# Kernel tuning notes

Hardware: AMD Instinct MI355X
Metric: run time of the kernel (lower is better)

Reference implementation:

```python
import jax, jax.numpy as jnp
import numpy as np

B, L, D = 32, 256, 128


def hard_sigmoid(x):
    # Keras-1 default inner_activation for LSTM gates
    return jnp.clip(0.2 * x + 0.5, 0.0, 1.0)


def lstm_step(x_t, h, c, W, U, b):
    # Keras-1 gate order: i, f, c(candidate), o
    z = x_t @ W + h @ U + b  # [B, 4D]
    d = h.shape[-1]
    i = hard_sigmoid(z[:, :d])
    f = hard_sigmoid(z[:, d:2 * d])
    g = jnp.tanh(z[:, 2 * d:3 * d])
    o = hard_sigmoid(z[:, 3 * d:])
    c_new = f * c + i * g
    h_new = o * jnp.tanh(c_new)
    return h_new, c_new


def setup_inputs() -> dict:
    key = jax.random.key(0)
    ks = jax.random.split(key, 9)
    s = 0.05  # weight scale to keep activations in a sane range
    return {
        "x": jax.random.normal(ks[0], (B, L, D), dtype=jnp.float32),
        "Wr": jax.random.normal(ks[1], (D, 4 * D), dtype=jnp.float32) * s,
        "Ur": jax.random.normal(ks[2], (D, 4 * D), dtype=jnp.float32) * s,
        "br": jnp.zeros((4 * D,), dtype=jnp.float32),
        "Ww": jax.random.normal(ks[3], (D, 4 * D), dtype=jnp.float32) * s,
        "Uw": jax.random.normal(ks[4], (D, 4 * D), dtype=jnp.float32) * s,
        "bw": jnp.zeros((4 * D,), dtype=jnp.float32),
        "Wc": jax.random.normal(ks[5], (2 * D, D), dtype=jnp.float32) * s,
        "bc": jnp.zeros((D,), dtype=jnp.float32),
    }


def reference(x, Wr, Ur, br, Ww, Uw, bw, Wc, bc):
    b, l, d = x.shape
    h0 = jnp.zeros((b, d), dtype=x.dtype)

    # ---- reader LSTM (return_sequences) ----
    def reader_step(carry, x_t):
        h, c = carry
        h, c = lstm_step(x_t, h, c, Wr, Ur, br)
        return (h, c), h

    _, o_seq = jax.lax.scan(reader_step, (h0, h0), jnp.swapaxes(x, 0, 1))  # [L, B, D]

    # ---- compose-and-write scan over timesteps ----
    mem0 = x  # read() sets mem_0 = input

    def write_step(carry, o_t):
        mem, h, c = carry  # mem: [B, L, D]
        # eq 2-3: attention over memory slots
        z = jax.nn.softmax(jnp.einsum('bd,bld->bl', o_t, mem), axis=-1)  # [B, L]
        m_rt = jnp.einsum('bl,bld->bd', z, mem)  # [B, D]
        # eq 4: composer (linear activation)
        c_t = jnp.concatenate([o_t, m_rt], axis=-1) @ Wc + bc  # [B, D]
        # eq 5: writer LSTM step
        h, c = lstm_step(c_t, h, c, Ww, Uw, bw)
        # eq 6: soft overwrite of memory
        zc = z[:, :, None]
        mem = mem * (1.0 - zc) + h[:, None, :] * zc
        return (mem, h, c), h

    (_, _, _), hs = jax.lax.scan(write_step, (mem0, h0, h0), o_seq)
    # return_mode == 'last_output'
    return hs[-1]
```

## Files before the change

### kernel.cpp

```cpp
#include <hip/hip_runtime.h>
#include <stdint.h>


#define LL 256

typedef float v2f __attribute__((ext_vector_type(2)));

__device__ __forceinline__ float hsig(float x) { return fminf(fmaxf(fmaf(x, 0.2f, 0.5f), 0.f), 1.f); }
__device__ __forceinline__ float tanh_fast(float x) {
  x = fminf(fmaxf(x, -15.f), 15.f);
  float e = __expf(2.f * x);
  return (e - 1.f) / (e + 1.f);
}

__global__ __launch_bounds__(512) void wtrans_kernel(const float* __restrict__ src,
                                                     float* __restrict__ dst, int jshift) {
  int idx = blockIdx.x * 512 + threadIdx.x;
  int J = 1 << jshift;
  int k = idx >> jshift, j = idx & (J - 1);
  dst[(((size_t)(k >> 2) << jshift) + j) * 4 + (k & 3)] = src[idx];
}

__global__ __launch_bounds__(512) void pvw_gemm(const float* __restrict__ Wc,
                                                const float* __restrict__ Ww,
                                                float* __restrict__ PVw) {
  __shared__ float wrow[128];
  const int r = blockIdx.x, j = threadIdx.x;
  if (j < 128) wrow[j] = Wc[r * 128 + j];
  __syncthreads();
  float a = 0.f;
#pragma unroll 4
  for (int m = 0; m < 128; m++) a = fmaf(wrow[m], Ww[m * 512 + j], a);
  PVw[r * 512 + j] = a;
}

__global__ __launch_bounds__(512) void pz_kernel(const float* __restrict__ bc,
                                                 const float* __restrict__ Ww,
                                                 const float* __restrict__ bw,
                                                 float* __restrict__ pz) {
  __shared__ float b_s[128];
  const int j = threadIdx.x;
  if (j < 128) b_s[j] = bc[j];
  __syncthreads();
  float a = bw[j];
#pragma unroll 4
  for (int m = 0; m < 128; m++) a = fmaf(b_s[m], Ww[m * 512 + j], a);
  pz[j] = a;
}

__global__ __launch_bounds__(512) void xw_gemm(const float* __restrict__ x,
                                               const float4* __restrict__ WrT4,
                                               const float* __restrict__ br,
                                               float* __restrict__ XW) {
  alignas(16) __shared__ float xs[8][128];
  const int b = blockIdx.x >> 5, tg = blockIdx.x & 31, tid = threadIdx.x;
  const float* xg = x + ((size_t)b * LL + tg * 8) * 128;
  if (tid < 256) ((float4*)&xs[0][0])[tid] = ((const float4*)xg)[tid];
  __syncthreads();
  float acc[8];
#pragma unroll
  for (int r = 0; r < 8; r++) acc[r] = 0.f;
#pragma unroll 8
  for (int i4 = 0; i4 < 32; i4++) {
    float4 w4 = WrT4[i4 * 512 + tid];
#pragma unroll
    for (int r = 0; r < 8; r++) {
      float4 v = *(const float4*)&xs[r][4 * i4];
      acc[r] += w4.x * v.x + w4.y * v.y + w4.z * v.z + w4.w * v.w;
    }
  }
  const float brj = br[tid];
  float* o = XW + ((size_t)b * LL + tg * 8) * 512;
#pragma unroll
  for (int r = 0; r < 8; r++) o[r * 512 + tid] = acc[r] + brj;
}

__global__ __launch_bounds__(512, 2) void reader_kernel(const float4* __restrict__ UrT4,
                                                        const float* __restrict__ XW,
                                                        float* __restrict__ og) {
  alignas(16) __shared__ float h_s[128];
  alignas(16) __shared__ float pp_s[512];
  const int b = blockIdx.x, tid = threadIdx.x;
  const float* XWb = XW + (size_t)b * LL * 512;
  float* ogb = og + (size_t)b * LL * 128;

  float4 U[32];
#pragma unroll
  for (int i4 = 0; i4 < 32; i4++) U[i4] = UrT4[i4 * 512 + tid];

  float c_r = 0.f;
  if (tid < 128) h_s[tid] = 0.f;
  float xwv = XWb[tid];
  __syncthreads();

  for (int t = 0; t < LL; t++) {
    float xw_n = (t + 1 < LL) ? XWb[(t + 1) * 512 + tid] : 0.f;
    v2f acc[4] = {{0.f, 0.f}, {0.f, 0.f}, {0.f, 0.f}, {0.f, 0.f}};
#pragma unroll
    for (int i4 = 0; i4 < 32; i4++) {
      float4 v = *(const float4*)&h_s[4 * i4];
      float4 w = U[i4];
      acc[i4 & 3] += (v2f){w.x, w.y} * (v2f){v.x, v.y};
      acc[i4 & 3] += (v2f){w.z, w.w} * (v2f){v.z, v.w};
    }
    v2f A = (acc[0] + acc[1]) + (acc[2] + acc[3]);
    pp_s[tid] = A.x + A.y + xwv;
    __syncthreads();
    if (tid < 128) {
      float zi = pp_s[tid], zf = pp_s[128 + tid], zg = pp_s[256 + tid], zo = pp_s[384 + tid];
      float ii = hsig(zi), ff = hsig(zf), gg = tanh_fast(zg), oo = hsig(zo);
      c_r = fmaf(ff, c_r, ii * gg);
      float h = oo * tanh_fast(c_r);
      h_s[tid] = h;
      ogb[t * 128 + tid] = h;
    }
    __syncthreads();
    xwv = xw_n;
  }
}

template <int NC>
__global__ __launch_bounds__(512, 2) void writer_kernel(
    const float* __restrict__ x,
    const float4* __restrict__ VwT4, const float4* __restrict__ UwT4,
    const float* __restrict__ og, const float* __restrict__ ZW,
    float* __restrict__ out) {
  alignas(16) __shared__ float h_s[128];
  alignas(16) __shared__ float osN[128];
  alignas(16) __shared__ float sc_s[256], ee_s[256];
  alignas(16) __shared__ float mr_s[128];
  alignas(16) __shared__ float pp_s[1024];
  __shared__ float rr_s[16];
  extern __shared__ float4 UwL[];

  const int b = blockIdx.x, tid = threadIdx.x;
  const int lane = tid & 63, wv = tid >> 6;
  const int l = tid >> 1, hf = tid & 1;
  const int q = tid >> 6, dp = tid & 63;

  const float* xg = x + (size_t)b * (LL * 128);
  const float* ogb = og + (size_t)b * (LL * 128);
  const float* ZWb = ZW + (size_t)b * (LL * 512);

  for (int i = tid; i < NC * 512; i += 512) UwL[i] = UwT4[i];

  v2f Mr[32], Mc[32];
#pragma unroll
  for (int w = 0; w < 32; w++) Mr[w] = *(const v2f*)(xg + l * 128 + hf * 64 + 2 * w);
#pragma unroll
  for (int i = 0; i < 32; i++) Mc[i] = *(const v2f*)(xg + (q * 32 + i) * 128 + 2 * dp);

  float c_w = 0.f;
  if (tid < 128) { h_s[tid] = 0.f; osN[tid] = ogb[tid]; }
  __syncthreads();
  {
    v2f S = {0.f, 0.f};
#pragma unroll
    for (int w = 0; w < 32; w++) S += Mr[w] * (*(const v2f*)&osN[hf * 64 + 2 * w]);
    float s = S.x + S.y;
    s += __shfl_xor(s, 1);
    if (hf == 0) sc_s[l] = s;
  }
  __syncthreads();

  float zwv = ZWb[tid];
  for (int t = 0; t < LL; t++) {
    const int tn = (t + 1 < LL) ? t + 1 : t;
    float zw_n = ZWb[(size_t)tn * 512 + tid];

    float huv;
    {
      v2f u0 = {0.f, 0.f}, u1 = {0.f, 0.f}, u2 = {0.f, 0.f}, u3 = {0.f, 0.f};
#pragma unroll 2
      for (int i4 = NC; i4 < 32; i4 += 2) {
        float4 w0 = UwT4[i4 * 512 + tid];
        float4 w1 = UwT4[(i4 + 1) * 512 + tid];
        float4 v0 = *(const float4*)&h_s[4 * i4];
        float4 v1 = *(const float4*)&h_s[4 * i4 + 4];
        u0 += (v2f){w0.x, w0.y} * (v2f){v0.x, v0.y};
        u0 += (v2f){w0.z, w0.w} * (v2f){v0.z, v0.w};
        u1 += (v2f){w1.x, w1.y} * (v2f){v1.x, v1.y};
        u1 += (v2f){w1.z, w1.w} * (v2f){v1.z, v1.w};
      }
#pragma unroll 2
      for (int i4 = 0; i4 < NC; i4++) {
        float4 w = UwL[i4 * 512 + tid];
        float4 v = *(const float4*)&h_s[4 * i4];
        u2 += (v2f){w.x, w.y} * (v2f){v.x, v.y};
        u3 += (v2f){w.z, w.w} * (v2f){v.z, v.w};
      }
      v2f U = (u0 + u1) + (u2 + u3);
      huv = U.x + U.y + zwv;
    }

    if (tid >= 128 && tid < 256 && t + 1 < LL)
      osN[tid - 128] = ogb[(t + 1) * 128 + (tid - 128)];
    if (tid < 256) {
      float s = sc_s[tid];
      float m = s;
#pragma unroll
      for (int off = 32; off > 0; off >>= 1) m = fmaxf(m, __shfl_xor(m, off));
      float e = __expf(s - m);
      ee_s[tid] = e;
      float s2 = e;
#pragma unroll
      for (int off = 32; off > 0; off >>= 1) s2 += __shfl_xor(s2, off);
      if (lane == 0) { rr_s[wv] = m; rr_s[8 + wv] = s2; }
    }
    __syncthreads();

    const float M = fmaxf(fmaxf(rr_s[0], rr_s[1]), fmaxf(rr_s[2], rr_s[3]));
    const float Sg = rr_s[8] * __expf(rr_s[0] - M) + rr_s[9] * __expf(rr_s[1] - M) +
                     rr_s[10] * __expf(rr_s[2] - M) + rr_s[11] * __expf(rr_s[3] - M);
    const float inv = 1.f / Sg;
    const float f = __expf(rr_s[tid >> 7] - M);
    const float fzi = f * inv;

    {
      v2f P0 = {0.f, 0.f}, P1 = {0.f, 0.f};
#pragma unroll
      for (int i = 0; i < 32; i += 2) {
        P0 += Mc[i] * ee_s[q * 32 + i];
        P1 += Mc[i + 1] * ee_s[q * 32 + i + 1];
      }
      v2f P = (P0 + P1) * f;
      *(v2f*)&pp_s[q * 128 + 2 * dp] = P;
    }
    __syncthreads();
    if (tid < 128) {
      float s = 0.f;
#pragma unroll
      for (int g8 = 0; g8 < 8; g8++) s += pp_s[g8 * 128 + tid];
      mr_s[tid] = s;
    }
    __syncthreads();
    {
      v2f a0 = {0.f, 0.f}, a1 = {0.f, 0.f}, a2 = {0.f, 0.f}, a3 = {0.f, 0.f};
#pragma unroll 2
      for (int i4 = 0; i4 < 32; i4 += 4) {
        float4 w0 = VwT4[i4 * 512 + tid];
        float4 w1 = VwT4[(i4 + 1) * 512 + tid];
        float4 w2 = VwT4[(i4 + 2) * 512 + tid];
        float4 w3 = VwT4[(i4 + 3) * 512 + tid];
        float4 v0 = *(const float4*)&mr_s[4 * i4];
        float4 v1 = *(const float4*)&mr_s[4 * i4 + 4];
        float4 v2 = *(const float4*)&mr_s[4 * i4 + 8];
        float4 v3 = *(const float4*)&mr_s[4 * i4 + 12];
        a0 += (v2f){w0.x, w0.y} * (v2f){v0.x, v0.y};
        a0 += (v2f){w0.z, w0.w} * (v2f){v0.z, v0.w};
        a1 += (v2f){w1.x, w1.y} * (v2f){v1.x, v1.y};
        a1 += (v2f){w1.z, w1.w} * (v2f){v1.z, v1.w};
        a2 += (v2f){w2.x, w2.y} * (v2f){v2.x, v2.y};
        a2 += (v2f){w2.z, w2.w} * (v2f){v2.z, v2.w};
        a3 += (v2f){w3.x, w3.y} * (v2f){v3.x, v3.y};
        a3 += (v2f){w3.z, w3.w} * (v2f){v3.z, v3.w};
      }
      v2f A = (a0 + a2) + (a1 + a3);
      pp_s[tid] = fmaf(A.x + A.y, inv, huv);
    }
    __syncthreads();
    if (tid < 128) {
      float zi = pp_s[tid], zf = pp_s[128 + tid], zg = pp_s[256 + tid], zo = pp_s[384 + tid];
      float ii = hsig(zi), ff = hsig(zf), gg = tanh_fast(zg), oo = hsig(zo);
      c_w = fmaf(ff, c_w, ii * gg);
      h_s[tid] = oo * tanh_fast(c_w);
    }
    __syncthreads();
    if (t + 1 < LL) {
      const float zr = ee_s[l] * fzi;
      v2f S0v = {0.f, 0.f}, S1v = {0.f, 0.f};
#pragma unroll
      for (int w = 0; w < 32; w += 2) {
        v2f h2a = *(const v2f*)&h_s[hf * 64 + 2 * w];
        v2f ma = Mr[w];
        v2f na = ma + (h2a - ma) * zr;
        Mr[w] = na;
        S0v += na * (*(const v2f*)&osN[hf * 64 + 2 * w]);
        v2f h2b = *(const v2f*)&h_s[hf * 64 + 2 * (w + 1)];
        v2f mb = Mr[w + 1];
        v2f nb = mb + (h2b - mb) * zr;
        Mr[w + 1] = nb;
        S1v += nb * (*(const v2f*)&osN[hf * 64 + 2 * (w + 1)]);
      }
      v2f Sv = S0v + S1v;
      float s = Sv.x + Sv.y;
      s += __shfl_xor(s, 1);
      if (hf == 0) sc_s[l] = s;
      v2f hc = *(const v2f*)&h_s[2 * dp];
#pragma unroll
      for (int i = 0; i < 32; i++) {
        float zc = ee_s[q * 32 + i] * fzi;
        v2f m = Mc[i];
        Mc[i] = m + (hc - m) * zc;
      }
    }
    __syncthreads();
    zwv = zw_n;
  }

  if (tid < 128) out[b * 128 + tid] = h_s[tid];
}

extern "C" void kernel_launch(void* const* d_in, const int* in_sizes, int n_in,
                              void* d_out, int out_size, void* d_ws, size_t ws_size,
                              hipStream_t stream) {
  const float* x  = (const float*)d_in[0];
  const float* Wr = (const float*)d_in[1];
  const float* Ur = (const float*)d_in[2];
  const float* br = (const float*)d_in[3];
  const float* Ww = (const float*)d_in[4];
  const float* Uw = (const float*)d_in[5];
  const float* bw = (const float*)d_in[6];
  const float* Wc = (const float*)d_in[7];
  const float* bc = (const float*)d_in[8];
  float* out = (float*)d_out;

  float* og  = (float*)d_ws;
  float* XW  = og + 1048576;
  float* WrT = XW + 4194304;
  float* UrT = WrT + 65536;
  float* UwT = UrT + 65536;
  float* PVw = UwT + 65536;
  float* PwT = PVw + 131072;
  float* VwT = PwT + 65536;
  float* pz  = VwT + 65536;

  static int nc_cached = -1;
  if (nc_cached < 0) {
    int want = 18 * 512 * (int)sizeof(float4);
    nc_cached = (hipFuncSetAttribute(
                     reinterpret_cast<const void*>(&writer_kernel<18>),
                     hipFuncAttributeMaxDynamicSharedMemorySize, want) == hipSuccess)
                    ? 18
                    : 6;
  }

  wtrans_kernel<<<128, 512, 0, stream>>>(Wr, WrT, 9);
  wtrans_kernel<<<128, 512, 0, stream>>>(Ur, UrT, 9);
  wtrans_kernel<<<128, 512, 0, stream>>>(Uw, UwT, 9);
  pvw_gemm<<<256, 512, 0, stream>>>(Wc, Ww, PVw);
  pz_kernel<<<1, 512, 0, stream>>>(bc, Ww, bw, pz);
  wtrans_kernel<<<128, 512, 0, stream>>>(PVw, PwT, 9);
  wtrans_kernel<<<128, 512, 0, stream>>>(PVw + 65536, VwT, 9);
  xw_gemm<<<1024, 512, 0, stream>>>(x, (const float4*)WrT, br, XW);
  reader_kernel<<<32, 512, 0, stream>>>((const float4*)UrT, XW, og);
  xw_gemm<<<1024, 512, 0, stream>>>(og, (const float4*)PwT, pz, XW);
  if (nc_cached == 18) {
    writer_kernel<18><<<32, 512, 18 * 512 * sizeof(float4), stream>>>(
        x, (const float4*)VwT, (const float4*)UwT, og, XW, out);
  } else {
    writer_kernel<6><<<32, 512, 6 * 512 * sizeof(float4), stream>>>(
        x, (const float4*)VwT, (const float4*)UwT, og, XW, out);
  }
}
```

Baseline: 2.030 ms.

## Move writer memory into padded LDS and keep Uw weights in registers

The writer kernel used to hold the memory matrix twice in registers (a row-major copy and a column-major copy) and kept part of Uw in LDS. It now stores one copy of the memory in dynamic LDS with a padded stride of 130, which frees the registers so the full Uw slice per thread can live in 32 float4 registers. The softmax is also restructured into a two-pass global max, which removes the per-group rescale factors. The trade-off is extra LDS traffic on every timestep for the memory reads and writes, plus one additional barrier, with a fallback kernel kept for cases where the LDS allocation fails.

```diff
diff --git a/kernel.cpp b/kernel.cpp
--- a/kernel.cpp
+++ b/kernel.cpp
@@ -3,6 +3,7 @@
 
 
 #define LL 256
+#define MS 130
 
 typedef float v2f __attribute__((ext_vector_type(2)));
 
@@ -119,8 +120,7 @@
   }
 }
 
-template <int NC>
-__global__ __launch_bounds__(512, 2) void writer_kernel(
+__global__ __launch_bounds__(512, 2) void writer_mem_lds(
     const float* __restrict__ x,
     const float4* __restrict__ VwT4, const float4* __restrict__ UwT4,
     const float* __restrict__ og, const float* __restrict__ ZW,
@@ -131,7 +131,7 @@
   alignas(16) __shared__ float mr_s[128];
   alignas(16) __shared__ float pp_s[1024];
   __shared__ float rr_s[16];
-  extern __shared__ float4 UwL[];
+  extern __shared__ float memL[];
 
   const int b = blockIdx.x, tid = threadIdx.x;
   const int lane = tid & 63, wv = tid >> 6;
@@ -142,21 +142,24 @@
   const float* ogb = og + (size_t)b * (LL * 128);
   const float* ZWb = ZW + (size_t)b * (LL * 512);
 
-  for (int i = tid; i < NC * 512; i += 512) UwL[i] = UwT4[i];
-
-  v2f Mr[32], Mc[32];
-#pragma unroll
-  for (int w = 0; w < 32; w++) Mr[w] = *(const v2f*)(xg + l * 128 + hf * 64 + 2 * w);
-#pragma unroll
-  for (int i = 0; i < 32; i++) Mc[i] = *(const v2f*)(xg + (q * 32 + i) * 128 + 2 * dp);
+  float4 UW[32];
+#pragma unroll
+  for (int i4 = 0; i4 < 32; i4++) UW[i4] = UwT4[i4 * 512 + tid];
+
+  for (int idx = tid; idx < 16384; idx += 512) {
+    int row = idx >> 6, c2 = (idx & 63) << 1;
+    *(v2f*)&memL[row * MS + c2] = *(const v2f*)&xg[(row << 7) + c2];
+  }
 
   float c_w = 0.f;
   if (tid < 128) { h_s[tid] = 0.f; osN[tid] = ogb[tid]; }
   __syncthreads();
   {
+    const float* mrow = &memL[l * MS + hf * 64];
     v2f S = {0.f, 0.f};
 #pragma unroll
-    for (int w = 0; w < 32; w++) S += Mr[w] * (*(const v2f*)&osN[hf * 64 + 2 * w]);
+    for (int w = 0; w < 32; w++)
+      S += (*(const v2f*)&mrow[2 * w]) * (*(const v2f*)&osN[hf * 64 + 2 * w]);
     float s = S.x + S.y;
     s += __shfl_xor(s, 1);
     if (hf == 0) sc_s[l] = s;
@@ -170,60 +173,47 @@
 
     float huv;
     {
-      v2f u0 = {0.f, 0.f}, u1 = {0.f, 0.f}, u2 = {0.f, 0.f}, u3 = {0.f, 0.f};
-#pragma unroll 2
-      for (int i4 = NC; i4 < 32; i4 += 2) {
-        float4 w0 = UwT4[i4 * 512 + tid];
-        float4 w1 = UwT4[(i4 + 1) * 512 + tid];
-        float4 v0 = *(const float4*)&h_s[4 * i4];
-        float4 v1 = *(const float4*)&h_s[4 * i4 + 4];
-        u0 += (v2f){w0.x, w0.y} * (v2f){v0.x, v0.y};
-        u0 += (v2f){w0.z, w0.w} * (v2f){v0.z, v0.w};
-        u1 += (v2f){w1.x, w1.y} * (v2f){v1.x, v1.y};
-        u1 += (v2f){w1.z, w1.w} * (v2f){v1.z, v1.w};
-      }
-#pragma unroll 2
-      for (int i4 = 0; i4 < NC; i4++) {
-        float4 w = UwL[i4 * 512 + tid];
+      v2f acc[4] = {{0.f, 0.f}, {0.f, 0.f}, {0.f, 0.f}, {0.f, 0.f}};
+#pragma unroll
+      for (int i4 = 0; i4 < 32; i4++) {
         float4 v = *(const float4*)&h_s[4 * i4];
-        u2 += (v2f){w.x, w.y} * (v2f){v.x, v.y};
-        u3 += (v2f){w.z, w.w} * (v2f){v.z, v.w};
-      }
-      v2f U = (u0 + u1) + (u2 + u3);
-      huv = U.x + U.y + zwv;
+        float4 w = UW[i4];
+        acc[i4 & 3] += (v2f){w.x, w.y} * (v2f){v.x, v.y};
+        acc[i4 & 3] += (v2f){w.z, w.w} * (v2f){v.z, v.w};
+      }
+      v2f A = (acc[0] + acc[1]) + (acc[2] + acc[3]);
+      huv = A.x + A.y + zwv;
     }
 
     if (tid >= 128 && tid < 256 && t + 1 < LL)
       osN[tid - 128] = ogb[(t + 1) * 128 + (tid - 128)];
     if (tid < 256) {
-      float s = sc_s[tid];
-      float m = s;
+      float m = sc_s[tid];
 #pragma unroll
       for (int off = 32; off > 0; off >>= 1) m = fmaxf(m, __shfl_xor(m, off));
-      float e = __expf(s - m);
+      if (lane == 0) rr_s[wv] = m;
+    }
+    __syncthreads();
+    if (tid < 256) {
+      float mx = fmaxf(fmaxf(rr_s[0], rr_s[1]), fmaxf(rr_s[2], rr_s[3]));
+      float e = __expf(sc_s[tid] - mx);
       ee_s[tid] = e;
       float s2 = e;
 #pragma unroll
       for (int off = 32; off > 0; off >>= 1) s2 += __shfl_xor(s2, off);
-      if (lane == 0) { rr_s[wv] = m; rr_s[8 + wv] = s2; }
-    }
-    __syncthreads();
-
-    const float M = fmaxf(fmaxf(rr_s[0], rr_s[1]), fmaxf(rr_s[2], rr_s[3]));
-    const float Sg = rr_s[8] * __expf(rr_s[0] - M) + rr_s[9] * __expf(rr_s[1] - M) +
-                     rr_s[10] * __expf(rr_s[2] - M) + rr_s[11] * __expf(rr_s[3] - M);
-    const float inv = 1.f / Sg;
-    const float f = __expf(rr_s[tid >> 7] - M);
-    const float fzi = f * inv;
-
+      if (lane == 0) rr_s[8 + wv] = s2;
+    }
+    __syncthreads();
+    const float inv = 1.f / (rr_s[8] + rr_s[9] + rr_s[10] + rr_s[11]);
     {
+      const float* mcol = &memL[(q * 32) * MS + 2 * dp];
       v2f P0 = {0.f, 0.f}, P1 = {0.f, 0.f};
 #pragma unroll
       for (int i = 0; i < 32; i += 2) {
-        P0 += Mc[i] * ee_s[q * 32 + i];
-        P1 += Mc[i + 1] * ee_s[q * 32 + i + 1];
-      }
-      v2f P = (P0 + P1) * f;
+        P0 += (*(const v2f*)&mcol[i * MS]) * ee_s[q * 32 + i];
+        P1 += (*(const v2f*)&mcol[(i + 1) * MS]) * ee_s[q * 32 + i + 1];
+      }
+      v2f P = P0 + P1;
       *(v2f*)&pp_s[q * 128 + 2 * dp] = P;
     }
     __syncthreads();
@@ -231,7 +221,7 @@
       float s = 0.f;
 #pragma unroll
       for (int g8 = 0; g8 < 8; g8++) s += pp_s[g8 * 128 + tid];
-      mr_s[tid] = s;
+      mr_s[tid] = s * inv;
     }
     __syncthreads();
     {
@@ -256,7 +246,7 @@
         a3 += (v2f){w3.z, w3.w} * (v2f){v3.z, v3.w};
       }
       v2f A = (a0 + a2) + (a1 + a3);
-      pp_s[tid] = fmaf(A.x + A.y, inv, huv);
+      pp_s[tid] = A.x + A.y + huv;
     }
     __syncthreads();
     if (tid < 128) {
@@ -267,7 +257,176 @@
     }
     __syncthreads();
     if (t + 1 < LL) {
-      const float zr = ee_s[l] * fzi;
+      const float zr = ee_s[l] * inv;
+      float* mrow = &memL[l * MS + hf * 64];
+      v2f S0v = {0.f, 0.f}, S1v = {0.f, 0.f};
+#pragma unroll
+      for (int w = 0; w < 32; w += 2) {
+        v2f h2a = *(const v2f*)&h_s[hf * 64 + 2 * w];
+        v2f ma = *(const v2f*)&mrow[2 * w];
+        v2f na = ma + (h2a - ma) * zr;
+        *(v2f*)&mrow[2 * w] = na;
+        S0v += na * (*(const v2f*)&osN[hf * 64 + 2 * w]);
+        v2f h2b = *(const v2f*)&h_s[hf * 64 + 2 * (w + 1)];
+        v2f mb = *(const v2f*)&mrow[2 * (w + 1)];
+        v2f nb = mb + (h2b - mb) * zr;
+        *(v2f*)&mrow[2 * (w + 1)] = nb;
+        S1v += nb * (*(const v2f*)&osN[hf * 64 + 2 * (w + 1)]);
+      }
+      v2f Sv = S0v + S1v;
+      float s = Sv.x + Sv.y;
+      s += __shfl_xor(s, 1);
+      if (hf == 0) sc_s[l] = s;
+    }
+    __syncthreads();
+    zwv = zw_n;
+  }
+
+  if (tid < 128) out[b * 128 + tid] = h_s[tid];
+}
+
+template <int NC>
+__global__ __launch_bounds__(512, 2) void writer_fb(
+    const float* __restrict__ x,
+    const float4* __restrict__ VwT4, const float4* __restrict__ UwT4,
+    const float* __restrict__ og, const float* __restrict__ ZW,
+    float* __restrict__ out) {
+  alignas(16) __shared__ float h_s[128];
+  alignas(16) __shared__ float osN[128];
+  alignas(16) __shared__ float sc_s[256], ee_s[256];
+  alignas(16) __shared__ float mr_s[128];
+  alignas(16) __shared__ float pp_s[1024];
+  __shared__ float rr_s[16];
+  extern __shared__ float4 UwL[];
+
+  const int b = blockIdx.x, tid = threadIdx.x;
+  const int lane = tid & 63, wv = tid >> 6;
+  const int l = tid >> 1, hf = tid & 1;
+  const int q = tid >> 6, dp = tid & 63;
+
+  const float* xg = x + (size_t)b * (LL * 128);
+  const float* ogb = og + (size_t)b * (LL * 128);
+  const float* ZWb = ZW + (size_t)b * (LL * 512);
+
+  for (int i = tid; i < NC * 512; i += 512) UwL[i] = UwT4[i];
+
+  v2f Mr[32], Mc[32];
+#pragma unroll
+  for (int w = 0; w < 32; w++) Mr[w] = *(const v2f*)(xg + l * 128 + hf * 64 + 2 * w);
+#pragma unroll
+  for (int i = 0; i < 32; i++) Mc[i] = *(const v2f*)(xg + (q * 32 + i) * 128 + 2 * dp);
+
+  float c_w = 0.f;
+  if (tid < 128) { h_s[tid] = 0.f; osN[tid] = ogb[tid]; }
+  __syncthreads();
+  {
+    v2f S = {0.f, 0.f};
+#pragma unroll
+    for (int w = 0; w < 32; w++) S += Mr[w] * (*(const v2f*)&osN[hf * 64 + 2 * w]);
+    float s = S.x + S.y;
+    s += __shfl_xor(s, 1);
+    if (hf == 0) sc_s[l] = s;
+  }
+  __syncthreads();
+
+  for (int t = 0; t < LL; t++) {
+    float huv;
+    {
+      float zwv = ZWb[(size_t)t * 512 + tid];
+      v2f u0 = {0.f, 0.f}, u1 = {0.f, 0.f}, u2 = {0.f, 0.f}, u3 = {0.f, 0.f};
+#pragma unroll 2
+      for (int i4 = NC; i4 < 32; i4 += 2) {
+        float4 w0 = UwT4[i4 * 512 + tid];
+        float4 w1 = UwT4[(i4 + 1) * 512 + tid];
+        float4 v0 = *(const float4*)&h_s[4 * i4];
+        float4 v1 = *(const float4*)&h_s[4 * i4 + 4];
+        u0 += (v2f){w0.x, w0.y} * (v2f){v0.x, v0.y};
+        u0 += (v2f){w0.z, w0.w} * (v2f){v0.z, v0.w};
+        u1 += (v2f){w1.x, w1.y} * (v2f){v1.x, v1.y};
+        u1 += (v2f){w1.z, w1.w} * (v2f){v1.z, v1.w};
+      }
+#pragma unroll 2
+      for (int i4 = 0; i4 < NC; i4++) {
+        float4 w = UwL[i4 * 512 + tid];
+        float4 v = *(const float4*)&h_s[4 * i4];
+        u2 += (v2f){w.x, w.y} * (v2f){v.x, v.y};
+        u3 += (v2f){w.z, w.w} * (v2f){v.z, v.w};
+      }
+      v2f U = (u0 + u1) + (u2 + u3);
+      huv = U.x + U.y + zwv;
+    }
+    if (tid >= 128 && tid < 256 && t + 1 < LL)
+      osN[tid - 128] = ogb[(t + 1) * 128 + (tid - 128)];
+    if (tid < 256) {
+      float m = sc_s[tid];
+#pragma unroll
+      for (int off = 32; off > 0; off >>= 1) m = fmaxf(m, __shfl_xor(m, off));
+      if (lane == 0) rr_s[wv] = m;
+    }
+    __syncthreads();
+    if (tid < 256) {
+      float mx = fmaxf(fmaxf(rr_s[0], rr_s[1]), fmaxf(rr_s[2], rr_s[3]));
+      float e = __expf(sc_s[tid] - mx);
+      ee_s[tid] = e;
+      float s2 = e;
+#pragma unroll
+      for (int off = 32; off > 0; off >>= 1) s2 += __shfl_xor(s2, off);
+      if (lane == 0) rr_s[8 + wv] = s2;
+    }
+    __syncthreads();
+    const float inv = 1.f / (rr_s[8] + rr_s[9] + rr_s[10] + rr_s[11]);
+    {
+      v2f P0 = {0.f, 0.f}, P1 = {0.f, 0.f};
+#pragma unroll
+      for (int i = 0; i < 32; i += 2) {
+        P0 += Mc[i] * ee_s[q * 32 + i];
+        P1 += Mc[i + 1] * ee_s[q * 32 + i + 1];
+      }
+      v2f P = P0 + P1;
+      *(v2f*)&pp_s[q * 128 + 2 * dp] = P;
+    }
+    __syncthreads();
+    if (tid < 128) {
+      float s = 0.f;
+#pragma unroll
+      for (int g8 = 0; g8 < 8; g8++) s += pp_s[g8 * 128 + tid];
+      mr_s[tid] = s * inv;
+    }
+    __syncthreads();
+    {
+      v2f a0 = {0.f, 0.f}, a1 = {0.f, 0.f}, a2 = {0.f, 0.f}, a3 = {0.f, 0.f};
+#pragma unroll 2
+      for (int i4 = 0; i4 < 32; i4 += 4) {
+        float4 w0 = VwT4[i4 * 512 + tid];
+        float4 w1 = VwT4[(i4 + 1) * 512 + tid];
+        float4 w2 = VwT4[(i4 + 2) * 512 + tid];
+        float4 w3 = VwT4[(i4 + 3) * 512 + tid];
+        float4 v0 = *(const float4*)&mr_s[4 * i4];
+        float4 v1 = *(const float4*)&mr_s[4 * i4 + 4];
+        float4 v2 = *(const float4*)&mr_s[4 * i4 + 8];
+        float4 v3 = *(const float4*)&mr_s[4 * i4 + 12];
+        a0 += (v2f){w0.x, w0.y} * (v2f){v0.x, v0.y};
+        a0 += (v2f){w0.z, w0.w} * (v2f){v0.z, v0.w};
+        a1 += (v2f){w1.x, w1.y} * (v2f){v1.x, v1.y};
+        a1 += (v2f){w1.z, w1.w} * (v2f){v1.z, v1.w};
+        a2 += (v2f){w2.x, w2.y} * (v2f){v2.x, v2.y};
+        a2 += (v2f){w2.z, w2.w} * (v2f){v2.z, v2.w};
+        a3 += (v2f){w3.x, w3.y} * (v2f){v3.x, v3.y};
+        a3 += (v2f){w3.z, w3.w} * (v2f){v3.z, v3.w};
+      }
+      v2f A = (a0 + a2) + (a1 + a3);
+      pp_s[tid] = A.x + A.y + huv;
+    }
+    __syncthreads();
+    if (tid < 128) {
+      float zi = pp_s[tid], zf = pp_s[128 + tid], zg = pp_s[256 + tid], zo = pp_s[384 + tid];
+      float ii = hsig(zi), ff = hsig(zf), gg = tanh_fast(zg), oo = hsig(zo);
+      c_w = fmaf(ff, c_w, ii * gg);
+      h_s[tid] = oo * tanh_fast(c_w);
+    }
+    __syncthreads();
+    if (t + 1 < LL) {
+      const float zr = ee_s[l] * inv;
       v2f S0v = {0.f, 0.f}, S1v = {0.f, 0.f};
 #pragma unroll
       for (int w = 0; w < 32; w += 2) {
@@ -289,13 +448,12 @@
       v2f hc = *(const v2f*)&h_s[2 * dp];
 #pragma unroll
       for (int i = 0; i < 32; i++) {
-        float zc = ee_s[q * 32 + i] * fzi;
+        float zc = ee_s[q * 32 + i] * inv;
         v2f m = Mc[i];
         Mc[i] = m + (hc - m) * zc;
       }
     }
     __syncthreads();
-    zwv = zw_n;
   }
 
   if (tid < 128) out[b * 128 + tid] = h_s[tid];
@@ -325,14 +483,14 @@
   float* VwT = PwT + 65536;
   float* pz  = VwT + 65536;
 
-  static int nc_cached = -1;
-  if (nc_cached < 0) {
-    int want = 18 * 512 * (int)sizeof(float4);
-    nc_cached = (hipFuncSetAttribute(
-                     reinterpret_cast<const void*>(&writer_kernel<18>),
-                     hipFuncAttributeMaxDynamicSharedMemorySize, want) == hipSuccess)
-                    ? 18
-                    : 6;
+  static int mode_cached = -1;
+  if (mode_cached < 0) {
+    int want = 256 * MS * (int)sizeof(float);
+    mode_cached = (hipFuncSetAttribute(
+                       reinterpret_cast<const void*>(&writer_mem_lds),
+                       hipFuncAttributeMaxDynamicSharedMemorySize, want) == hipSuccess)
+                      ? 1
+                      : 0;
   }
 
   wtrans_kernel<<<128, 512, 0, stream>>>(Wr, WrT, 9);
@@ -345,11 +503,11 @@
   xw_gemm<<<1024, 512, 0, stream>>>(x, (const float4*)WrT, br, XW);
   reader_kernel<<<32, 512, 0, stream>>>((const float4*)UrT, XW, og);
   xw_gemm<<<1024, 512, 0, stream>>>(og, (const float4*)PwT, pz, XW);
-  if (nc_cached == 18) {
-    writer_kernel<18><<<32, 512, 18 * 512 * sizeof(float4), stream>>>(
+  if (mode_cached == 1) {
+    writer_mem_lds<<<32, 512, 256 * MS * sizeof(float), stream>>>(
         x, (const float4*)VwT, (const float4*)UwT, og, XW, out);
   } else {
-    writer_kernel<6><<<32, 512, 6 * 512 * sizeof(float4), stream>>>(
+    writer_fb<6><<<32, 512, 6 * 512 * sizeof(float4), stream>>>(
         x, (const float4*)VwT, (const float4*)UwT, og, XW, out);
   }
 }
```

After: 3.246 ms. +59.9%, slower.
